# Performance work log

Hardware: AMD Instinct MI355X
Metric: run time of the kernel (lower is better)

The kernel has to match this reference:

```python
import jax, jax.numpy as jnp
import numpy as np

B, N, S, D = 2, 2048, 2048, 256
NHEAD = 4
HDIM = D // NHEAD
EPS = 1e-5


def embed_rotary(x, cos, sin):
    # x, cos, sin: [B,N,D]; rotate pairs (even, odd)
    x2 = jnp.stack([-x[..., 1::2], x[..., ::2]], axis=-1).reshape(x.shape)
    return x * cos + x2 * sin


def layernorm(x, g, b):
    mu = jnp.mean(x, axis=-1, keepdims=True)
    var = jnp.var(x, axis=-1, keepdims=True)
    return (x - mu) * jax.lax.rsqrt(var + EPS) * g + b


def setup_inputs() -> dict:
    key = jax.random.key(0)
    ks = jax.random.split(key, 10)
    w = 0.05
    return {
        "x": jax.random.normal(ks[0], (B, N, D), jnp.float32),
        "source": jax.random.normal(ks[1], (B, S, D), jnp.float32),
        "x_pe": jax.random.normal(ks[2], (B, N, D, 2), jnp.float32),
        "source_pe": jax.random.normal(ks[3], (B, S, D, 2), jnp.float32),
        "Wq": jax.random.normal(ks[4], (D, D), jnp.float32) * w,
        "Wk": jax.random.normal(ks[5], (D, D), jnp.float32) * w,
        "Wv": jax.random.normal(ks[6], (D, D), jnp.float32) * w,
        "Wm": jax.random.normal(ks[7], (D, D), jnp.float32) * w,
        "W1": jax.random.normal(ks[8], (2 * D, 2 * D), jnp.float32) * w,
        "W2": jax.random.normal(ks[9], (2 * D, D), jnp.float32) * w,
        "g1": jnp.ones((D,), jnp.float32),
        "b1": jnp.zeros((D,), jnp.float32),
        "g2": jnp.ones((D,), jnp.float32),
        "b2": jnp.zeros((D,), jnp.float32),
    }


def reference(x, source, x_pe, source_pe, Wq, Wk, Wv, Wm, W1, W2, g1, b1, g2, b2):
    bs = x.shape[0]
    # projections (no bias)
    qw = x @ Wq            # [B,N,D]
    kw = source @ Wk       # [B,S,D]
    vw = source @ Wv       # [B,S,D]
    # inline rotary PE applied before head split
    qw = embed_rotary(qw, x_pe[..., 0], x_pe[..., 1])
    kw = embed_rotary(kw, source_pe[..., 0], source_pe[..., 1])
    qw = qw.reshape(bs, -1, NHEAD, HDIM)
    kw = kw.reshape(bs, -1, NHEAD, HDIM)
    vw = vw.reshape(bs, -1, NHEAD, HDIM)
    # attention (no mask)
    a = jnp.einsum('nlhd,nshd->nlsh', qw, kw) / jnp.sqrt(jnp.float32(HDIM))
    a = jax.nn.softmax(a, axis=2)
    o = jnp.einsum('nlsh,nshd->nlhd', a, vw).reshape(bs, -1, NHEAD * HDIM)
    message = layernorm(o @ Wm, g1, b1)
    h = jax.nn.relu(jnp.concatenate([x, message], axis=2) @ W1)
    message = layernorm(h @ W2, g2, b2)
    return x + message
```

## Files before the change

kernel.cpp:

```cpp
#include <hip/hip_runtime.h>
#include <hip/hip_bf16.h>

#define NN 2048
#define DD 256
#define HD 64
#define LN_EPS 1e-5f
#define SPLIT 4
#define CHUNK (NN / SPLIT)
#define KVB 64

typedef __bf16 bf16x8 __attribute__((ext_vector_type(8)));
typedef __bf16 bf16x4 __attribute__((ext_vector_type(4)));
typedef float  f32x4  __attribute__((ext_vector_type(4)));

static __device__ __forceinline__ bf16x8 make8(bf16x4 lo, bf16x4 hi) {
    return bf16x8{lo[0],lo[1],lo[2],lo[3],hi[0],hi[1],hi[2],hi[3]};
}
static __device__ __forceinline__ bf16x8 ldfrag(const __bf16* p) {
    bf16x4 lo = *(const bf16x4*)p;
    bf16x4 hi = *(const bf16x4*)(p + 16);
    return make8(lo, hi);
}

static __device__ __forceinline__ void stage64(const __bf16* __restrict__ g, int ldg,
                                               __bf16* lds, int t) {
    const int w = t >> 6, lane = t & 63;
    #pragma unroll
    for (int i = 0; i < 2; ++i) {
        int chunk = (w + 4*i) * 64 + lane;
        int r = chunk >> 3;
        int j = (chunk & 7) ^ (r & 7);
        __builtin_amdgcn_global_load_lds(
            (const __attribute__((address_space(1))) void*)(g + (long)r * ldg + j * 8),
            (__attribute__((address_space(3))) void*)(lds + (w + 4*i) * 512),
            16, 0, 0);
    }
}
static __device__ __forceinline__ bf16x8 ldfrag_swz(const __bf16* lds, int row, int cbyte) {
    const char* p = (const char*)(lds + row * 64);
    int sw = (row & 7) << 4;
    bf16x4 lo = *(const bf16x4*)(p + (cbyte ^ sw));
    bf16x4 hi = *(const bf16x4*)(p + ((cbyte + 32) ^ sw));
    return make8(lo, hi);
}

__global__ void wtall_kernel(const float* __restrict__ Wq, const float* __restrict__ Wk,
                             const float* __restrict__ Wv, const float* __restrict__ Wm,
                             const float* __restrict__ W1, const float* __restrict__ W2,
                             const float* __restrict__ x,  const float* __restrict__ src,
                             __bf16* __restrict__ Wqt, __bf16* __restrict__ Wkvt,
                             __bf16* __restrict__ Wmt, __bf16* __restrict__ W1t,
                             __bf16* __restrict__ W2t, __bf16* __restrict__ xb,
                             __bf16* __restrict__ srcb)
{
    int i = blockIdx.x * 256 + threadIdx.x;
    if (i < 65536) {
        int n = i >> 8, k = i & 255;
        Wqt[i] = (__bf16)Wq[k * 256 + n];
    } else if (i < 196608) {
        int j = i - 65536;
        int n = j >> 8, k = j & 255;
        Wkvt[j] = (__bf16)(n < 256 ? Wk[k * 256 + n] : Wv[k * 256 + n - 256]);
    } else if (i < 262144) {
        int j = i - 196608;
        int n = j >> 8, k = j & 255;
        Wmt[j] = (__bf16)Wm[k * 256 + n];
    } else if (i < 524288) {
        int j = i - 262144;
        int n = j >> 9, k = j & 511;
        W1t[j] = (__bf16)W1[k * 512 + n];
    } else if (i < 655360) {
        int j = i - 524288;
        int n = j >> 9, k = j & 511;
        W2t[j] = (__bf16)W2[k * 256 + n];
    } else if (i < 786432) {
        int j = i - 655360;
        const float4* p = (const float4*)&x[(long)j * 8];
        float4 a0 = p[0], a1 = p[1];
        *(bf16x8*)&xb[(long)j * 8] = bf16x8{
            (__bf16)a0.x,(__bf16)a0.y,(__bf16)a0.z,(__bf16)a0.w,
            (__bf16)a1.x,(__bf16)a1.y,(__bf16)a1.z,(__bf16)a1.w};
    } else if (i < 917504) {
        int j = i - 786432;
        const float4* p = (const float4*)&src[(long)j * 8];
        float4 a0 = p[0], a1 = p[1];
        *(bf16x8*)&srcb[(long)j * 8] = bf16x8{
            (__bf16)a0.x,(__bf16)a0.y,(__bf16)a0.z,(__bf16)a0.w,
            (__bf16)a1.x,(__bf16)a1.y,(__bf16)a1.z,(__bf16)a1.w};
    }
}

template<int EPI>
__global__ __launch_bounds__(256) void gemm2_kernel(
    const __bf16* __restrict__ A1, const __bf16* __restrict__ A2,
    const __bf16* __restrict__ B1, const __bf16* __restrict__ B2,
    void* __restrict__ C1, void* __restrict__ C2, void* __restrict__ C3,
    const float* __restrict__ pe1, const float* __restrict__ pe2,
    int M, int N, int K)
{
    __shared__ alignas(16) __bf16 As[64 * 64];
    __shared__ alignas(16) __bf16 Bs[64 * 64];

    const int t = threadIdx.x;
    const int rowbase = blockIdx.y * 64;
    const int w = t >> 6, lane = t & 63;
    const int wr = w >> 1, wc = w & 1;
    const int lr = lane & 15, lg = lane >> 4;

    const __bf16* Ap = A1;
    const __bf16* Bp = B1;
    const float*  pe = pe1;
    int colbase = blockIdx.x * 64;
    bool isQ = true;
    if (EPI == 5) {
        isQ = blockIdx.x < 4;
        if (!isQ) { Ap = A2; Bp = B2; pe = pe2; colbase = (blockIdx.x - 4) * 64; }
    }

    f32x4 acc[2][2] = {};

    for (int kb = 0; kb < K; kb += 64) {
        __syncthreads();
        stage64(Ap + (long)rowbase * K + kb, K, As, t);
        stage64(Bp + (long)colbase * K + kb, K, Bs, t);
        __syncthreads();

        #pragma unroll
        for (int kk = 0; kk < 2; ++kk) {
            bf16x8 af[2], bfr[2];
            #pragma unroll
            for (int mt = 0; mt < 2; ++mt)
                af[mt] = ldfrag_swz(As, wr*32 + mt*16 + lr, kk*64 + lg*8);
            #pragma unroll
            for (int nt = 0; nt < 2; ++nt)
                bfr[nt] = ldfrag_swz(Bs, wc*32 + nt*16 + lr, kk*64 + lg*8);
            #pragma unroll
            for (int mt = 0; mt < 2; ++mt)
                #pragma unroll
                for (int nt = 0; nt < 2; ++nt)
                    acc[mt][nt] = __builtin_amdgcn_mfma_f32_16x16x32_bf16(af[mt], bfr[nt], acc[mt][nt], 0, 0, 0);
        }
    }

    #pragma unroll
    for (int mt = 0; mt < 2; ++mt) {
        #pragma unroll
        for (int nt = 0; nt < 2; ++nt) {
            #pragma unroll
            for (int r = 0; r < 4; ++r) {
                long grow = rowbase + wr*32 + mt*16 + lg*4 + r;
                int  gcol = colbase + wc*32 + nt*16 + lr;
                float val = acc[mt][nt][r];
                if (EPI == 2) {
                    ((float*)C1)[grow * N + gcol] = val;
                } else if (EPI == 3) {
                    ((__bf16*)C1)[grow * N + gcol] = (__bf16)fmaxf(val, 0.f);
                } else {
                    if (isQ || gcol < 256) {
                        float partner = __shfl_xor(val, 1);
                        const float* pp = &pe[(grow * DD + gcol) * 2];
                        float c = pp[0], s = pp[1];
                        val = (gcol & 1) ? (val * c + partner * s) : (val * c - partner * s);
                        ((__bf16*)(isQ ? C1 : C2))[grow * DD + gcol] = (__bf16)val;
                    } else {
                        ((__bf16*)C3)[grow * DD + gcol - 256] = (__bf16)val;
                    }
                }
            }
        }
    }
}

__global__ __launch_bounds__(256) void attn_part_kernel(
    const __bf16* __restrict__ q, const __bf16* __restrict__ kk,
    const __bf16* __restrict__ v, float* __restrict__ op, float* __restrict__ ml)
{
    __shared__ alignas(16) __bf16 Qs[64 * 64];
    __shared__ alignas(16) __bf16 Ks[64 * 64];
    __shared__ alignas(16) __bf16 Vt[64][72];
    __shared__ alignas(16) __bf16 Ps[4][16][72];

    const int t = threadIdx.x;
    const int qb = blockIdx.x * 64;
    const int h  = blockIdx.y;
    const int z  = blockIdx.z;
    const int b  = z >> 2, sp = z & 3;
    const int w = t >> 6, lane = t & 63;
    const int lr = lane & 15, lg = lane >> 4;
    const long row0 = (long)b * NN;

    stage64(q + (row0 + qb) * DD + h * HD, DD, Qs, t);
    __syncthreads();
    bf16x8 qf[2];
    qf[0] = ldfrag_swz(Qs, w*16 + lr, lg*8);
    qf[1] = ldfrag_swz(Qs, w*16 + lr, 64 + lg*8);

    f32x4 acco[4] = {};
    float mrun[4], lrun[4];
    #pragma unroll
    for (int r = 0; r < 4; ++r) { mrun[r] = -INFINITY; lrun[r] = 0.f; }

    const int sr = t >> 2, scc = (t & 3) * 16;
    for (int sb = sp * CHUNK; sb < sp * CHUNK + CHUNK; sb += KVB) {
        __syncthreads();
        stage64(kk + (row0 + sb) * DD + h * HD, DD, Ks, t);
        {
            const __bf16* vp = &v[(row0 + sb + sr) * DD + h * HD + scc];
            bf16x8 v0 = *(const bf16x8*)vp;
            bf16x8 v1 = *(const bf16x8*)(vp + 8);
            #pragma unroll
            for (int j = 0; j < 8; ++j) {
                int hd = scc + j;
                Vt[hd][sr ^ (4 * ((hd >> 3) & 7))] = v0[j];
                int hd2 = scc + 8 + j;
                Vt[hd2][sr ^ (4 * ((hd2 >> 3) & 7))] = v1[j];
            }
        }
        __syncthreads();

        f32x4 accs[4] = {};
        #pragma unroll
        for (int nt = 0; nt < 4; ++nt)
            #pragma unroll
            for (int ks = 0; ks < 2; ++ks) {
                bf16x8 kf = ldfrag_swz(Ks, nt*16 + lr, ks*64 + lg*8);
                accs[nt] = __builtin_amdgcn_mfma_f32_16x16x32_bf16(qf[ks], kf, accs[nt], 0, 0, 0);
            }

        float sc[4];
        #pragma unroll
        for (int r = 0; r < 4; ++r) {
            float s0 = accs[0][r] * 0.125f, s1 = accs[1][r] * 0.125f;
            float s2 = accs[2][r] * 0.125f, s3 = accs[3][r] * 0.125f;
            float mx = fmaxf(fmaxf(s0, s1), fmaxf(s2, s3));
            #pragma unroll
            for (int m = 1; m < 16; m <<= 1) mx = fmaxf(mx, __shfl_xor(mx, m));
            float mnew = fmaxf(mrun[r], mx);
            float p0 = __expf(s0 - mnew), p1 = __expf(s1 - mnew);
            float p2 = __expf(s2 - mnew), p3 = __expf(s3 - mnew);
            float rs = (p0 + p1) + (p2 + p3);
            #pragma unroll
            for (int m = 1; m < 16; m <<= 1) rs += __shfl_xor(rs, m);
            sc[r] = __expf(mrun[r] - mnew);
            lrun[r] = lrun[r] * sc[r] + rs;
            mrun[r] = mnew;
            Ps[w][lg*4 + r][lr]      = (__bf16)p0;
            Ps[w][lg*4 + r][lr + 16] = (__bf16)p1;
            Ps[w][lg*4 + r][lr + 32] = (__bf16)p2;
            Ps[w][lg*4 + r][lr + 48] = (__bf16)p3;
        }
        asm volatile("s_waitcnt lgkmcnt(0)" ::: "memory");
        __builtin_amdgcn_sched_barrier(0);

        bf16x8 pf[2];
        pf[0] = ldfrag(&Ps[w][lr][4*lg]);
        pf[1] = ldfrag(&Ps[w][lr][32 + 4*lg]);

        #pragma unroll
        for (int nt = 0; nt < 4; ++nt) {
            #pragma unroll
            for (int r = 0; r < 4; ++r) acco[nt][r] *= sc[r];
            int d = nt*16 + lr;
            int xsw = 4 * ((d >> 3) & 7);
            const __bf16* vrow = &Vt[d][0];
            #pragma unroll
            for (int ks = 0; ks < 2; ++ks) {
                bf16x4 lo = *(const bf16x4*)&vrow[(ks*32 + 4*lg) ^ xsw];
                bf16x4 hi = *(const bf16x4*)&vrow[(ks*32 + 16 + 4*lg) ^ xsw];
                acco[nt] = __builtin_amdgcn_mfma_f32_16x16x32_bf16(pf[ks], make8(lo, hi), acco[nt], 0, 0, 0);
            }
        }
    }

    long pr = (long)(sp * 2 + b) * 2048 + qb + w*16 + lg*4;
    #pragma unroll
    for (int nt = 0; nt < 4; ++nt)
        #pragma unroll
        for (int r = 0; r < 4; ++r)
            op[(pr + r) * 256 + h * HD + nt*16 + lr] = acco[nt][r];
    if (lr == 0) {
        #pragma unroll
        for (int r = 0; r < 4; ++r) {
            long mi = ((long)(sp * 2 + b) * 4 + h) * 2048 + (qb + w*16 + lg*4 + r);
            *(float2*)&ml[mi * 2] = make_float2(mrun[r], lrun[r]);
        }
    }
}

__global__ __launch_bounds__(256) void attn_comb_kernel(
    const float* __restrict__ op, const float* __restrict__ ml, __bf16* __restrict__ o)
{
    int row = blockIdx.x;
    int t = threadIdx.x;
    int b = row >> 11, n = row & 2047;
    int h = t >> 6;
    float m[SPLIT], l[SPLIT];
    #pragma unroll
    for (int sp = 0; sp < SPLIT; ++sp) {
        float2 v2 = *(const float2*)&ml[(((long)(sp*2 + b) * 4 + h) * 2048 + n) * 2];
        m[sp] = v2.x; l[sp] = v2.y;
    }
    float M = fmaxf(fmaxf(m[0], m[1]), fmaxf(m[2], m[3]));
    float L = 0.f, oa = 0.f;
    #pragma unroll
    for (int sp = 0; sp < SPLIT; ++sp) {
        float wgt = __expf(m[sp] - M);
        L  += l[sp] * wgt;
        oa += op[((long)(sp*2 + b) * 2048 + n) * 256 + t] * wgt;
    }
    o[(long)row * 256 + t] = (__bf16)(oa / L);
}

__global__ __launch_bounds__(256) void ln1_cat_kernel(
    const float* __restrict__ m1, const float* __restrict__ x,
    const float* __restrict__ g, const float* __restrict__ bb,
    __bf16* __restrict__ cat)
{
    __shared__ float red[2][4];
    int row = blockIdx.x, t = threadIdx.x;
    float val = m1[(long)row * DD + t];
    float s = val, sq = val * val;
    #pragma unroll
    for (int m = 1; m < 64; m <<= 1) { s += __shfl_xor(s, m); sq += __shfl_xor(sq, m); }
    int w = t >> 6;
    if ((t & 63) == 0) { red[0][w] = s; red[1][w] = sq; }
    __syncthreads();
    s  = red[0][0] + red[0][1] + red[0][2] + red[0][3];
    sq = red[1][0] + red[1][1] + red[1][2] + red[1][3];
    float mean = s * (1.f / DD);
    float var  = sq * (1.f / DD) - mean * mean;
    float y = (val - mean) * rsqrtf(var + LN_EPS) * g[t] + bb[t];
    cat[(long)row * 512 + 256 + t] = (__bf16)y;
    cat[(long)row * 512 + t]       = (__bf16)x[(long)row * DD + t];
}

__global__ __launch_bounds__(256) void ln2_res_kernel(
    const float* __restrict__ m2, const float* __restrict__ x,
    const float* __restrict__ g, const float* __restrict__ bb,
    float* __restrict__ out)
{
    __shared__ float red[2][4];
    int row = blockIdx.x, t = threadIdx.x;
    float val = m2[(long)row * DD + t];
    float s = val, sq = val * val;
    #pragma unroll
    for (int m = 1; m < 64; m <<= 1) { s += __shfl_xor(s, m); sq += __shfl_xor(sq, m); }
    int w = t >> 6;
    if ((t & 63) == 0) { red[0][w] = s; red[1][w] = sq; }
    __syncthreads();
    s  = red[0][0] + red[0][1] + red[0][2] + red[0][3];
    sq = red[1][0] + red[1][1] + red[1][2] + red[1][3];
    float mean = s * (1.f / DD);
    float var  = sq * (1.f / DD) - mean * mean;
    float y = (val - mean) * rsqrtf(var + LN_EPS) * g[t] + bb[t];
    out[(long)row * DD + t] = x[(long)row * DD + t] + y;
}

extern "C" void kernel_launch(void* const* d_in, const int* in_sizes, int n_in,
                              void* d_out, int out_size, void* d_ws, size_t ws_size,
                              hipStream_t stream)
{
    const float* x   = (const float*)d_in[0];
    const float* src = (const float*)d_in[1];
    const float* xpe = (const float*)d_in[2];
    const float* spe = (const float*)d_in[3];
    const float* Wq  = (const float*)d_in[4];
    const float* Wk  = (const float*)d_in[5];
    const float* Wv  = (const float*)d_in[6];
    const float* Wm  = (const float*)d_in[7];
    const float* W1  = (const float*)d_in[8];
    const float* W2  = (const float*)d_in[9];
    const float* g1  = (const float*)d_in[10];
    const float* b1  = (const float*)d_in[11];
    const float* g2  = (const float*)d_in[12];
    const float* b2  = (const float*)d_in[13];

    char* ws = (char*)d_ws;
    size_t off = 0;
    auto alloc = [&](size_t bytes) -> void* {
        void* p = ws + off; off += (bytes + 255) & ~(size_t)255; return p;
    };
    __bf16* Wqt  = (__bf16*)alloc(256 * 256 * 2);
    __bf16* Wkvt = (__bf16*)alloc(512 * 256 * 2);
    __bf16* Wmt  = (__bf16*)alloc(256 * 256 * 2);
    __bf16* W1t  = (__bf16*)alloc(512 * 512 * 2);
    __bf16* W2t  = (__bf16*)alloc(256 * 512 * 2);
    __bf16* xb   = (__bf16*)alloc((size_t)4096 * 256 * 2);
    __bf16* srcb = (__bf16*)alloc((size_t)4096 * 256 * 2);
    __bf16* qws  = (__bf16*)alloc((size_t)4096 * 256 * 2);
    __bf16* kws  = (__bf16*)alloc((size_t)4096 * 256 * 2);
    __bf16* vws  = (__bf16*)alloc((size_t)4096 * 256 * 2);
    __bf16* ows  = (__bf16*)alloc((size_t)4096 * 256 * 2);
    char*   big  = (char*)alloc((size_t)16 * 1024 * 1024);
    float*  op   = (float*)big;
    float*  m1   = (float*)big;
    __bf16* cat  = (__bf16*)(big + (size_t)4  * 1024 * 1024);
    __bf16* hws  = (__bf16*)(big + (size_t)8  * 1024 * 1024);
    float*  m2   = (float*)(big + (size_t)12 * 1024 * 1024);
    float*  ml   = (float*)alloc((size_t)SPLIT * 2 * 4 * 2048 * 2 * 4);

    wtall_kernel<<<3584, 256, 0, stream>>>(Wq, Wk, Wv, Wm, W1, W2, x, src,
                                           Wqt, Wkvt, Wmt, W1t, W2t, xb, srcb);

    gemm2_kernel<5><<<dim3(12, 64), 256, 0, stream>>>(
        xb, srcb, Wqt, Wkvt, qws, kws, vws, xpe, spe, 4096, 256, 256);

    attn_part_kernel<<<dim3(32, 4, 2 * SPLIT), 256, 0, stream>>>(qws, kws, vws, op, ml);
    attn_comb_kernel<<<4096, 256, 0, stream>>>(op, ml, ows);

    gemm2_kernel<2><<<dim3(4, 64), 256, 0, stream>>>(
        ows, nullptr, Wmt, nullptr, m1, nullptr, nullptr, nullptr, nullptr, 4096, 256, 256);
    ln1_cat_kernel<<<4096, 256, 0, stream>>>(m1, x, g1, b1, cat);
    gemm2_kernel<3><<<dim3(8, 64), 256, 0, stream>>>(
        cat, nullptr, W1t, nullptr, hws, nullptr, nullptr, nullptr, nullptr, 4096, 512, 512);
    gemm2_kernel<2><<<dim3(4, 64), 256, 0, stream>>>(
        hws, nullptr, W2t, nullptr, m2, nullptr, nullptr, nullptr, nullptr, 4096, 256, 512);
    ln2_res_kernel<<<4096, 256, 0, stream>>>(m2, x, g2, b2, (float*)d_out);
}
```

Measured before the change: 187.6 us.

## Fuse output GEMMs with LayerNorm epilogues and double attention split-K

Adds a gemm_ln kernel in which each 16-row block computes all 256 output columns, so LayerNorm can be done in the epilogue. It replaces the Wm GEMM plus ln1_cat and the W2 GEMM plus ln2_res, which removes the fp32 intermediate round trips and two launches. The attention KV split goes from 4 to 8, giving more blocks for occupancy at the cost of a larger partial buffer and more combine work. Q staging and the P buffer now share LDS to reduce shared-memory use. The fused GEMM launches only 256 blocks and has little reuse of the B operand per block, which may limit throughput.

```diff
diff --git a/kernel.cpp b/kernel.cpp
--- a/kernel.cpp
+++ b/kernel.cpp
@@ -5,7 +5,7 @@
 #define DD 256
 #define HD 64
 #define LN_EPS 1e-5f
-#define SPLIT 4
+#define SPLIT 8
 #define CHUNK (NN / SPLIT)
 #define KVB 64
 
@@ -151,9 +151,7 @@
                 long grow = rowbase + wr*32 + mt*16 + lg*4 + r;
                 int  gcol = colbase + wc*32 + nt*16 + lr;
                 float val = acc[mt][nt][r];
-                if (EPI == 2) {
-                    ((float*)C1)[grow * N + gcol] = val;
-                } else if (EPI == 3) {
+                if (EPI == 3) {
                     ((__bf16*)C1)[grow * N + gcol] = (__bf16)fmaxf(val, 0.f);
                 } else {
                     if (isQ || gcol < 256) {
@@ -171,29 +169,117 @@
     }
 }
 
+template<int MODE>
+__global__ __launch_bounds__(256) void gemm_ln_kernel(
+    const __bf16* __restrict__ A, const __bf16* __restrict__ Bt,
+    const __bf16* __restrict__ xb, const float* __restrict__ xf,
+    const float* __restrict__ g, const float* __restrict__ bb,
+    void* __restrict__ out, int K)
+{
+    __shared__ alignas(16) __bf16 As[16 * 64];
+    __shared__ alignas(16) __bf16 Bs[256 * 64];
+    __shared__ float red[2][4][16];
+
+    const int t = threadIdx.x;
+    const int w = t >> 6, lane = t & 63;
+    const int lr = lane & 15, lg = lane >> 4;
+    const int rowbase = blockIdx.x * 16;
+
+    f32x4 acc[4] = {};
+    for (int kb = 0; kb < K; kb += 64) {
+        __syncthreads();
+        if (w < 2) {
+            int c = w * 64 + lane;
+            int r = c >> 3, j = (c & 7) ^ (r & 7);
+            __builtin_amdgcn_global_load_lds(
+                (const __attribute__((address_space(1))) void*)(A + (long)(rowbase + r) * K + kb + j * 8),
+                (__attribute__((address_space(3))) void*)(As + w * 512),
+                16, 0, 0);
+        }
+        #pragma unroll
+        for (int i = 0; i < 8; ++i) {
+            int c = (w + 4 * i) * 64 + lane;
+            int r = c >> 3, j = (c & 7) ^ (r & 7);
+            __builtin_amdgcn_global_load_lds(
+                (const __attribute__((address_space(1))) void*)(Bt + (long)r * K + kb + j * 8),
+                (__attribute__((address_space(3))) void*)(Bs + (w + 4 * i) * 512),
+                16, 0, 0);
+        }
+        __syncthreads();
+        #pragma unroll
+        for (int kk = 0; kk < 2; ++kk) {
+            bf16x8 af = ldfrag_swz(As, lr, kk*64 + lg*8);
+            #pragma unroll
+            for (int nt = 0; nt < 4; ++nt) {
+                bf16x8 bf = ldfrag_swz(Bs, w*64 + nt*16 + lr, kk*64 + lg*8);
+                acc[nt] = __builtin_amdgcn_mfma_f32_16x16x32_bf16(af, bf, acc[nt], 0, 0, 0);
+            }
+        }
+    }
+
+    #pragma unroll
+    for (int r = 0; r < 4; ++r) {
+        float s = 0.f, q = 0.f;
+        #pragma unroll
+        for (int nt = 0; nt < 4; ++nt) { float v_ = acc[nt][r]; s += v_; q += v_ * v_; }
+        #pragma unroll
+        for (int m = 1; m < 16; m <<= 1) { s += __shfl_xor(s, m); q += __shfl_xor(q, m); }
+        if (lr == 0) { red[0][w][lg*4 + r] = s; red[1][w][lg*4 + r] = q; }
+    }
+    __syncthreads();
+    #pragma unroll
+    for (int r = 0; r < 4; ++r) {
+        int lrow = lg*4 + r;
+        float s = red[0][0][lrow] + red[0][1][lrow] + red[0][2][lrow] + red[0][3][lrow];
+        float q = red[1][0][lrow] + red[1][1][lrow] + red[1][2][lrow] + red[1][3][lrow];
+        float mean = s * (1.f / 256.f);
+        float var  = q * (1.f / 256.f) - mean * mean;
+        float inv  = rsqrtf(var + LN_EPS);
+        long grow = rowbase + lrow;
+        #pragma unroll
+        for (int nt = 0; nt < 4; ++nt) {
+            int col = w*64 + nt*16 + lr;
+            float y = (acc[nt][r] - mean) * inv * g[col] + bb[col];
+            if (MODE == 0) {
+                ((__bf16*)out)[grow * 512 + 256 + col] = (__bf16)y;
+            } else {
+                ((float*)out)[grow * 256 + col] = xf[grow * 256 + col] + y;
+            }
+        }
+    }
+    if (MODE == 0) {
+        int r = t >> 4, c0 = (t & 15) * 16;
+        bf16x8 v0 = *(const bf16x8*)&xb[(long)(rowbase + r) * 256 + c0];
+        bf16x8 v1 = *(const bf16x8*)&xb[(long)(rowbase + r) * 256 + c0 + 8];
+        *(bf16x8*)&((__bf16*)out)[(long)(rowbase + r) * 512 + c0]     = v0;
+        *(bf16x8*)&((__bf16*)out)[(long)(rowbase + r) * 512 + c0 + 8] = v1;
+    }
+}
+
 __global__ __launch_bounds__(256) void attn_part_kernel(
     const __bf16* __restrict__ q, const __bf16* __restrict__ kk,
     const __bf16* __restrict__ v, float* __restrict__ op, float* __restrict__ ml)
 {
-    __shared__ alignas(16) __bf16 Qs[64 * 64];
+    __shared__ alignas(16) __bf16 QP[4 * 16 * 72];
     __shared__ alignas(16) __bf16 Ks[64 * 64];
     __shared__ alignas(16) __bf16 Vt[64][72];
-    __shared__ alignas(16) __bf16 Ps[4][16][72];
 
     const int t = threadIdx.x;
     const int qb = blockIdx.x * 64;
     const int h  = blockIdx.y;
     const int z  = blockIdx.z;
-    const int b  = z >> 2, sp = z & 3;
+    const int b  = z >> 3, sp = z & 7;
     const int w = t >> 6, lane = t & 63;
     const int lr = lane & 15, lg = lane >> 4;
     const long row0 = (long)b * NN;
 
-    stage64(q + (row0 + qb) * DD + h * HD, DD, Qs, t);
+    __bf16 (*Ps)[16][72] = (__bf16 (*)[16][72])QP;
+
+    stage64(q + (row0 + qb) * DD + h * HD, DD, QP, t);
     __syncthreads();
     bf16x8 qf[2];
-    qf[0] = ldfrag_swz(Qs, w*16 + lr, lg*8);
-    qf[1] = ldfrag_swz(Qs, w*16 + lr, 64 + lg*8);
+    qf[0] = ldfrag_swz(QP, w*16 + lr, lg*8);
+    qf[1] = ldfrag_swz(QP, w*16 + lr, 64 + lg*8);
 
     f32x4 acco[4] = {};
     float mrun[4], lrun[4];
@@ -300,7 +386,9 @@
         float2 v2 = *(const float2*)&ml[(((long)(sp*2 + b) * 4 + h) * 2048 + n) * 2];
         m[sp] = v2.x; l[sp] = v2.y;
     }
-    float M = fmaxf(fmaxf(m[0], m[1]), fmaxf(m[2], m[3]));
+    float M = m[0];
+    #pragma unroll
+    for (int sp = 1; sp < SPLIT; ++sp) M = fmaxf(M, m[sp]);
     float L = 0.f, oa = 0.f;
     #pragma unroll
     for (int sp = 0; sp < SPLIT; ++sp) {
@@ -309,51 +397,6 @@
         oa += op[((long)(sp*2 + b) * 2048 + n) * 256 + t] * wgt;
     }
     o[(long)row * 256 + t] = (__bf16)(oa / L);
-}
-
-__global__ __launch_bounds__(256) void ln1_cat_kernel(
-    const float* __restrict__ m1, const float* __restrict__ x,
-    const float* __restrict__ g, const float* __restrict__ bb,
-    __bf16* __restrict__ cat)
-{
-    __shared__ float red[2][4];
-    int row = blockIdx.x, t = threadIdx.x;
-    float val = m1[(long)row * DD + t];
-    float s = val, sq = val * val;
-    #pragma unroll
-    for (int m = 1; m < 64; m <<= 1) { s += __shfl_xor(s, m); sq += __shfl_xor(sq, m); }
-    int w = t >> 6;
-    if ((t & 63) == 0) { red[0][w] = s; red[1][w] = sq; }
-    __syncthreads();
-    s  = red[0][0] + red[0][1] + red[0][2] + red[0][3];
-    sq = red[1][0] + red[1][1] + red[1][2] + red[1][3];
-    float mean = s * (1.f / DD);
-    float var  = sq * (1.f / DD) - mean * mean;
-    float y = (val - mean) * rsqrtf(var + LN_EPS) * g[t] + bb[t];
-    cat[(long)row * 512 + 256 + t] = (__bf16)y;
-    cat[(long)row * 512 + t]       = (__bf16)x[(long)row * DD + t];
-}
-
-__global__ __launch_bounds__(256) void ln2_res_kernel(
-    const float* __restrict__ m2, const float* __restrict__ x,
-    const float* __restrict__ g, const float* __restrict__ bb,
-    float* __restrict__ out)
-{
-    __shared__ float red[2][4];
-    int row = blockIdx.x, t = threadIdx.x;
-    float val = m2[(long)row * DD + t];
-    float s = val, sq = val * val;
-    #pragma unroll
-    for (int m = 1; m < 64; m <<= 1) { s += __shfl_xor(s, m); sq += __shfl_xor(sq, m); }
-    int w = t >> 6;
-    if ((t & 63) == 0) { red[0][w] = s; red[1][w] = sq; }
-    __syncthreads();
-    s  = red[0][0] + red[0][1] + red[0][2] + red[0][3];
-    sq = red[1][0] + red[1][1] + red[1][2] + red[1][3];
-    float mean = s * (1.f / DD);
-    float var  = sq * (1.f / DD) - mean * mean;
-    float y = (val - mean) * rsqrtf(var + LN_EPS) * g[t] + bb[t];
-    out[(long)row * DD + t] = x[(long)row * DD + t] + y;
 }
 
 extern "C" void kernel_launch(void* const* d_in, const int* in_sizes, int n_in,
@@ -391,13 +434,10 @@
     __bf16* kws  = (__bf16*)alloc((size_t)4096 * 256 * 2);
     __bf16* vws  = (__bf16*)alloc((size_t)4096 * 256 * 2);
     __bf16* ows  = (__bf16*)alloc((size_t)4096 * 256 * 2);
-    char*   big  = (char*)alloc((size_t)16 * 1024 * 1024);
-    float*  op   = (float*)big;
-    float*  m1   = (float*)big;
-    __bf16* cat  = (__bf16*)(big + (size_t)4  * 1024 * 1024);
-    __bf16* hws  = (__bf16*)(big + (size_t)8  * 1024 * 1024);
-    float*  m2   = (float*)(big + (size_t)12 * 1024 * 1024);
-    float*  ml   = (float*)alloc((size_t)SPLIT * 2 * 4 * 2048 * 2 * 4);
+    float*  op   = (float*) alloc((size_t)SPLIT * 2 * 2048 * 256 * 4);
+    float*  ml   = (float*) alloc((size_t)SPLIT * 2 * 4 * 2048 * 2 * 4);
+    __bf16* cat  = (__bf16*)alloc((size_t)4096 * 512 * 2);
+    __bf16* hws  = (__bf16*)alloc((size_t)4096 * 512 * 2);
 
     wtall_kernel<<<3584, 256, 0, stream>>>(Wq, Wk, Wv, Wm, W1, W2, x, src,
                                            Wqt, Wkvt, Wmt, W1t, W2t, xb, srcb);
@@ -408,12 +448,8 @@
     attn_part_kernel<<<dim3(32, 4, 2 * SPLIT), 256, 0, stream>>>(qws, kws, vws, op, ml);
     attn_comb_kernel<<<4096, 256, 0, stream>>>(op, ml, ows);
 
-    gemm2_kernel<2><<<dim3(4, 64), 256, 0, stream>>>(
-        ows, nullptr, Wmt, nullptr, m1, nullptr, nullptr, nullptr, nullptr, 4096, 256, 256);
-    ln1_cat_kernel<<<4096, 256, 0, stream>>>(m1, x, g1, b1, cat);
+    gemm_ln_kernel<0><<<256, 256, 0, stream>>>(ows, Wmt, xb, nullptr, g1, b1, cat, 256);
     gemm2_kernel<3><<<dim3(8, 64), 256, 0, stream>>>(
         cat, nullptr, W1t, nullptr, hws, nullptr, nullptr, nullptr, nullptr, 4096, 512, 512);
-    gemm2_kernel<2><<<dim3(4, 64), 256, 0, stream>>>(
-        hws, nullptr, W2t, nullptr, m2, nullptr, nullptr, nullptr, nullptr, 4096, 256, 512);
-    ln2_res_kernel<<<4096, 256, 0, stream>>>(m2, x, g2, b2, (float*)d_out);
-}
+    gemm_ln_kernel<1><<<256, 256, 0, stream>>>(hws, W2t, nullptr, x, g2, b2, d_out, 512);
+}
```

After: 182.8 us. -2.5%, faster.
